# Optimization experiments

Hardware: AMD Instinct MI355X
Metric: run time of the kernel (lower is better)

Reference implementation:

```python
import jax, jax.numpy as jnp
import numpy as np

B, H, W, C = 4, 64, 64, 256
DQK, DV = C // 8, C // 2  # 32, 128


def setup_inputs() -> dict:
    key = jax.random.key(0)
    ks = jax.random.split(key, 5)
    x = jax.random.normal(ks[0], (B, H, W, C), dtype=jnp.float32)
    # 1x1 conv kernels stored as [C_in, C_out] matrices (Glorot-ish scale)
    Wf = jax.random.normal(ks[1], (C, DQK), dtype=jnp.float32) * 0.05
    Wg = jax.random.normal(ks[2], (C, DQK), dtype=jnp.float32) * 0.05
    Wh = jax.random.normal(ks[3], (C, DV), dtype=jnp.float32) * 0.05
    Wv = jax.random.normal(ks[4], (DV, C), dtype=jnp.float32) * 0.05
    return {
        "x": x,
        "Wf": Wf, "bf": jnp.zeros((DQK,), jnp.float32),
        "Wg": Wg, "bg": jnp.zeros((DQK,), jnp.float32),
        "Wh": Wh, "bh": jnp.zeros((DV,), jnp.float32),
        "Wv": Wv, "bv": jnp.zeros((C,), jnp.float32),
    }


def reference(x, Wf, bf, Wg, bg, Wh, bh, Wv, bv):
    b, h, w, c = x.shape
    n = h * w
    xf = x.reshape(b, n, c)                       # flatten spatial dims
    f = xf @ Wf + bf                              # [b, n, dqk] keys
    g = xf @ Wg + bg                              # [b, n, dqk] queries
    v = xf @ Wh + bh                              # [b, n, dv]  values
    s = jnp.einsum('bnd,bmd->bnm', g, f)          # unscaled scores [b, n, n]
    beta = jax.nn.softmax(s, axis=-1)
    o = jnp.einsum('bnm,bmd->bnd', beta, v)       # [b, n, dv]
    o = o @ Wv + bv                               # output 1x1 conv -> [b, n, c]
    out = xf + o                                  # residual
    return out.reshape(b, h, w, c)
```

## Files before the change

kernel.cpp:

```cpp
#include <hip/hip_runtime.h>
#include <hip/hip_bf16.h>
#include <stdint.h>

typedef __attribute__((ext_vector_type(8))) short short8;
typedef __attribute__((ext_vector_type(4))) float f32x4;

#define B_   4
#define N_   4096
#define C_   256
#define DQK  32
#define DV   128
#define NCOL 192
#define QBLK 64
#define KVB  64
#define TOT  (B_*N_)
#define PROWB 144

__device__ __forceinline__ uint16_t f2bf(float f) {
    uint32_t u = __float_as_uint(f);
    u += 0x7fffu + ((u >> 16) & 1u);
    return (uint16_t)(u >> 16);
}

__global__ __launch_bounds__(256) void prep_weights(
    const float* __restrict__ Wf, const float* __restrict__ Wg,
    const float* __restrict__ Wh, const float* __restrict__ Wv,
    uint16_t* __restrict__ WfghT, uint16_t* __restrict__ WvT)
{
    int idx = blockIdx.x * 256 + threadIdx.x;
    if (idx < NCOL * C_) {
        int c = idx / C_, k = idx % C_;
        float v = (c < DQK)   ? Wf[k * DQK + c]
                : (c < 2*DQK) ? Wg[k * DQK + (c - DQK)]
                              : Wh[k * DV  + (c - 2*DQK)];
        WfghT[idx] = f2bf(v);
    }
    int idx2 = idx - NCOL * C_;
    if (idx2 >= 0 && idx2 < C_ * DV) {
        int c = idx2 / DV, k = idx2 % DV;
        WvT[idx2] = f2bf(Wv[k * C_ + c]);
    }
}

__global__ __launch_bounds__(256) void proj_kernel(
    const float* __restrict__ x, const uint16_t* __restrict__ WfghT,
    const float* __restrict__ bf, const float* __restrict__ bg,
    const float* __restrict__ bh,
    uint16_t* __restrict__ fK, uint16_t* __restrict__ gQ,
    uint16_t* __restrict__ vT)
{
    __shared__ __align__(16) uint16_t vlds[128 * 72];
    const int lane = threadIdx.x & 63;
    const int w    = threadIdx.x >> 6;
    const int rb   = blockIdx.x * 64 + w * 16;
    const int lr   = lane & 15, lg = lane >> 4;
    const int arow = rb + lr;

    const f32x4 z = {0.f, 0.f, 0.f, 0.f};
    f32x4 acc[12];
#pragma unroll
    for (int i = 0; i < 12; ++i) acc[i] = z;

#pragma unroll
    for (int kc = 0; kc < 8; ++kc) {
        const float* ap = x + (size_t)arow * C_ + kc * 32 + lg * 8;
        f32x4 u0 = *(const f32x4*)ap;
        f32x4 u1 = *(const f32x4*)(ap + 4);
        short8 a;
        a[0]=(short)f2bf(u0[0]); a[1]=(short)f2bf(u0[1]);
        a[2]=(short)f2bf(u0[2]); a[3]=(short)f2bf(u0[3]);
        a[4]=(short)f2bf(u1[0]); a[5]=(short)f2bf(u1[1]);
        a[6]=(short)f2bf(u1[2]); a[7]=(short)f2bf(u1[3]);
#pragma unroll
        for (int ct = 0; ct < 12; ++ct) {
            short8 b = *(const short8*)(WfghT + (ct*16 + lr) * C_ + kc*32 + lg*8);
            acc[ct] = __builtin_amdgcn_mfma_f32_16x16x32_bf16(a, b, acc[ct], 0, 0, 0);
        }
    }

#pragma unroll
    for (int ct = 0; ct < 12; ++ct) {
        int col = ct * 16 + lr;
        float bias = (col < DQK)   ? bf[col]
                   : (col < 2*DQK) ? bg[col - DQK]
                                   : bh[col - 2*DQK];
#pragma unroll
        for (int i = 0; i < 4; ++i) {
            int row = rb + lg * 4 + i;
            uint16_t h = f2bf(acc[ct][i] + bias);
            if (col < DQK) {
                fK[(size_t)row * DQK + col] = h;
            } else if (col < 2*DQK) {
                gQ[(size_t)row * DQK + (col - DQK)] = h;
            } else {
                int vc = col - 2*DQK;
                int nl = w * 16 + lg * 4 + i;
                vlds[vc * 72 + nl] = h;
            }
        }
    }
    __syncthreads();
    const int rb0   = blockIdx.x * 64;
    const int b_    = rb0 >> 12;
    const int nbase = rb0 & (N_ - 1);
    const int tid   = threadIdx.x;
#pragma unroll
    for (int pass = 0; pass < 4; ++pass) {
        int vc = pass * 32 + (tid >> 3);
        int nl = (tid & 7) * 8;
        short8 vv = *(const short8*)(vlds + vc * 72 + nl);
        *(short8*)(vT + ((size_t)b_ * DV + vc) * N_ + nbase + nl) = vv;
    }
}

template<int S>
__global__ __launch_bounds__(256) void attn_kernel(
    const uint16_t* __restrict__ fK, const uint16_t* __restrict__ gQ,
    const uint16_t* __restrict__ vT,
    float* __restrict__ opart, float* __restrict__ msplit,
    float* __restrict__ lsplit)
{
    __shared__ __align__(16) uint8_t lds[2*4096 + 2*16384 + 4*2304];
    uint8_t* Kl = lds;
    uint8_t* Vl = lds + 2*4096;
    const int lane = threadIdx.x & 63;
    const int w    = threadIdx.x >> 6;
    uint8_t* Pl = lds + 2*4096 + 2*16384 + w * 2304;
    const int lr = lane & 15, lg = lane >> 4;

    const int bid   = blockIdx.x;
    const int xcd   = bid & 7;
    const int b     = xcd >> 1;
    const int t_    = bid >> 3;
    const int s     = t_ >> 5;
    const int qtile = (xcd & 1) * 32 + (t_ & 31);
    const int qbase = qtile * QBLK;
    const int kv0   = s * (N_ / S);
    const int NTS   = 64 / S;

    short8 aq = *(const short8*)(gQ + ((size_t)(b*N_ + qbase + w*16 + lr)) * DQK + lg*8);

    const f32x4 z = {0.f, 0.f, 0.f, 0.f};
    f32x4 oa[8];
#pragma unroll
    for (int i = 0; i < 8; ++i) oa[i] = z;
    float m_run[4] = {-1e30f, -1e30f, -1e30f, -1e30f};
    float l_run[4] = {0.f, 0.f, 0.f, 0.f};

    const uint16_t* fbase = fK + (size_t)b * N_ * DQK;
    const uint16_t* vbase = vT + (size_t)b * DV * N_;

    auto STAGE = [&](int buf, int kbase) {
        {
            int sl  = w * 64 + lane;
            int key = sl >> 2;
            int g   = (sl & 3) ^ ((key >> 1) & 3);
            const uint16_t* src = fbase + (size_t)(kbase + key) * DQK + g * 8;
            __builtin_amdgcn_global_load_lds(
                (const __attribute__((address_space(1))) uint32_t*)src,
                (__attribute__((address_space(3))) uint32_t*)(Kl + buf*4096 + w*1024),
                16, 0, 0);
        }
#pragma unroll
        for (int q = 0; q < 4; ++q) {
            int sl = w * 256 + q * 64 + lane;
            int vc = sl >> 3;
            int ks = (sl & 7) ^ (vc & 7);
            const uint16_t* src = vbase + (size_t)vc * N_ + kbase + ks * 8;
            __builtin_amdgcn_global_load_lds(
                (const __attribute__((address_space(1))) uint32_t*)src,
                (__attribute__((address_space(3))) uint32_t*)(Vl + buf*16384 + (w*256 + q*64)*16),
                16, 0, 0);
        }
    };

    auto COMPUTE = [&](int buf) {
        const uint8_t* Kb = Kl + buf * 4096;
        const uint8_t* Vb = Vl + buf * 16384;
        f32x4 sf[4];
#pragma unroll
        for (int kg = 0; kg < 4; ++kg) {
            int key   = kg * 16 + lr;
            int slotK = key * 4 + (lg ^ ((key >> 1) & 3));
            short8 kb = *(const short8*)(Kb + slotK * 16);
            sf[kg] = __builtin_amdgcn_mfma_f32_16x16x32_bf16(aq, kb, z, 0, 0, 0);
        }
#pragma unroll
        for (int i = 0; i < 4; ++i) {
            float tm = fmaxf(fmaxf(sf[0][i], sf[1][i]), fmaxf(sf[2][i], sf[3][i]));
            tm = fmaxf(tm, __shfl_xor(tm, 1, 16));
            tm = fmaxf(tm, __shfl_xor(tm, 2, 16));
            tm = fmaxf(tm, __shfl_xor(tm, 4, 16));
            tm = fmaxf(tm, __shfl_xor(tm, 8, 16));
            float mn = fmaxf(m_run[i], tm);
            float sc = __expf(m_run[i] - mn);
            m_run[i] = mn;
            float rs = 0.f;
#pragma unroll
            for (int kg = 0; kg < 4; ++kg) {
                float p = __expf(sf[kg][i] - mn);
                sf[kg][i] = p;
                rs += p;
            }
            rs += __shfl_xor(rs, 1, 16);
            rs += __shfl_xor(rs, 2, 16);
            rs += __shfl_xor(rs, 4, 16);
            rs += __shfl_xor(rs, 8, 16);
            l_run[i] = l_run[i] * sc + rs;
#pragma unroll
            for (int ct = 0; ct < 8; ++ct) oa[ct][i] *= sc;
#pragma unroll
            for (int kg = 0; kg < 4; ++kg) {
                *(uint16_t*)(Pl + (lg*4 + i) * PROWB + (kg*16 + lr) * 2) = f2bf(sf[kg][i]);
            }
        }
        __builtin_amdgcn_sched_barrier(0);
        asm volatile("s_waitcnt lgkmcnt(0)" ::: "memory");
        __builtin_amdgcn_sched_barrier(0);
#pragma unroll
        for (int kc = 0; kc < 2; ++kc) {
            short8 pa = *(const short8*)(Pl + lr * PROWB + kc * 64 + lg * 16);
#pragma unroll
            for (int ct = 0; ct < 8; ++ct) {
                int vc    = ct * 16 + lr;
                int ks    = kc * 4 + lg;
                int slotV = vc * 8 + (ks ^ (vc & 7));
                short8 vb = *(const short8*)(Vb + slotV * 16);
                oa[ct] = __builtin_amdgcn_mfma_f32_16x16x32_bf16(pa, vb, oa[ct], 0, 0, 0);
            }
        }
    };

    STAGE(0, kv0);
    for (int t = 0; t < NTS; ++t) {
        if (t + 1 < NTS) {
            STAGE((t + 1) & 1, kv0 + (t + 1) * KVB);
            asm volatile("s_waitcnt vmcnt(5)" ::: "memory");
        } else {
            asm volatile("s_waitcnt vmcnt(0)" ::: "memory");
        }
        asm volatile("s_barrier" ::: "memory");
        COMPUTE(t & 1);
        asm volatile("s_barrier" ::: "memory");
    }

#pragma unroll
    for (int i = 0; i < 4; ++i) {
        int grow = b * N_ + qbase + w * 16 + lg * 4 + i;
        float* op = opart + ((size_t)s * TOT + grow) * DV;
#pragma unroll
        for (int ct = 0; ct < 8; ++ct) {
            op[ct * 16 + lr] = oa[ct][i];
        }
        if (lr == 0) {
            msplit[s * TOT + grow] = m_run[i];
            lsplit[s * TOT + grow] = l_run[i];
        }
    }
}

template<int S>
__global__ __launch_bounds__(256) void out_kernel(
    const float* __restrict__ opart, const float* __restrict__ msplit,
    const float* __restrict__ lsplit, const uint16_t* __restrict__ WvT,
    const float* __restrict__ x, const float* __restrict__ bv,
    float* __restrict__ out)
{
    const int lane = threadIdx.x & 63;
    const int w    = threadIdx.x >> 6;
    const int rb   = blockIdx.x * 64 + w * 16;
    const int lr   = lane & 15, lg = lane >> 4;
    const int row  = rb + lr;

    float wsn[S];
    {
        float ms[S], ls[S];
#pragma unroll
        for (int su = 0; su < S; ++su) {
            ms[su] = msplit[su * TOT + row];
            ls[su] = lsplit[su * TOT + row];
        }
        float mx = -1e30f;
#pragma unroll
        for (int su = 0; su < S; ++su) mx = fmaxf(mx, ms[su]);
        float L = 0.f;
#pragma unroll
        for (int su = 0; su < S; ++su) { wsn[su] = __expf(ms[su] - mx); L += wsn[su] * ls[su]; }
        float inv = 1.f / L;
#pragma unroll
        for (int su = 0; su < S; ++su) wsn[su] *= inv;
    }

    const f32x4 z = {0.f, 0.f, 0.f, 0.f};
    f32x4 acc[16];
#pragma unroll
    for (int i = 0; i < 16; ++i) acc[i] = z;

#pragma unroll
    for (int kc = 0; kc < 4; ++kc) {
        float af[8] = {0.f,0.f,0.f,0.f,0.f,0.f,0.f,0.f};
#pragma unroll
        for (int su = 0; su < S; ++su) {
            const float* ov = opart + ((size_t)su * TOT + row) * DV + kc*32 + lg*8;
            f32x4 o0 = *(const f32x4*)ov;
            f32x4 o1 = *(const f32x4*)(ov + 4);
#pragma unroll
            for (int j = 0; j < 4; ++j) {
                af[j]     += wsn[su] * o0[j];
                af[j + 4] += wsn[su] * o1[j];
            }
        }
        short8 a;
#pragma unroll
        for (int j = 0; j < 8; ++j) a[j] = (short)f2bf(af[j]);
#pragma unroll
        for (int ct = 0; ct < 16; ++ct) {
            short8 bfr = *(const short8*)(WvT + (ct*16 + lr) * DV + kc*32 + lg*8);
            acc[ct] = __builtin_amdgcn_mfma_f32_16x16x32_bf16(a, bfr, acc[ct], 0, 0, 0);
        }
    }
#pragma unroll
    for (int ct = 0; ct < 16; ++ct) {
        int col = ct * 16 + lr;
        float bb = bv[col];
#pragma unroll
        for (int i = 0; i < 4; ++i) {
            size_t idx = (size_t)(rb + lg*4 + i) * C_ + col;
            out[idx] = acc[ct][i] + bb + x[idx];
        }
    }
}

extern "C" void kernel_launch(void* const* d_in, const int* in_sizes, int n_in,
                              void* d_out, int out_size, void* d_ws, size_t ws_size,
                              hipStream_t stream)
{
    const float* x  = (const float*)d_in[0];
    const float* Wf = (const float*)d_in[1];
    const float* bf = (const float*)d_in[2];
    const float* Wg = (const float*)d_in[3];
    const float* bg = (const float*)d_in[4];
    const float* Wh = (const float*)d_in[5];
    const float* bh = (const float*)d_in[6];
    const float* Wv = (const float*)d_in[7];
    const float* bv = (const float*)d_in[8];
    float* out = (float*)d_out;

    const size_t fixed = (size_t)NCOL*C_*2 + (size_t)C_*DV*2
                       + 2*(size_t)TOT*DQK*2 + (size_t)B_*DV*N_*2;
    auto need = [&](size_t S){ return fixed + S*TOT*DV*4 + 2*S*TOT*4; };
    const int S = (ws_size >= need(4)) ? 4 : (ws_size >= need(2)) ? 2 : 1;

    uint8_t* ws = (uint8_t*)d_ws;
    size_t off = 0;
    uint16_t* WfghT = (uint16_t*)(ws + off); off += (size_t)NCOL * C_ * 2;
    uint16_t* WvT   = (uint16_t*)(ws + off); off += (size_t)C_ * DV * 2;
    uint16_t* fK    = (uint16_t*)(ws + off); off += (size_t)TOT * DQK * 2;
    uint16_t* gQ    = (uint16_t*)(ws + off); off += (size_t)TOT * DQK * 2;
    uint16_t* vT    = (uint16_t*)(ws + off); off += (size_t)B_ * DV * N_ * 2;
    float*    opart = (float*)(ws + off);    off += (size_t)S * TOT * DV * 4;
    float*    mspl  = (float*)(ws + off);    off += (size_t)S * TOT * 4;
    float*    lspl  = (float*)(ws + off);    off += (size_t)S * TOT * 4;

    prep_weights<<<320, 256, 0, stream>>>(Wf, Wg, Wh, Wv, WfghT, WvT);
    proj_kernel <<<256, 256, 0, stream>>>(x, WfghT, bf, bg, bh, fK, gQ, vT);
    switch (S) {
    case 4:
        attn_kernel<4><<<1024, 256, 0, stream>>>(fK, gQ, vT, opart, mspl, lspl);
        out_kernel<4> <<<256, 256, 0, stream>>>(opart, mspl, lspl, WvT, x, bv, out);
        break;
    case 2:
        attn_kernel<2><<<512, 256, 0, stream>>>(fK, gQ, vT, opart, mspl, lspl);
        out_kernel<2> <<<256, 256, 0, stream>>>(opart, mspl, lspl, WvT, x, bv, out);
        break;
    default:
        attn_kernel<1><<<256, 256, 0, stream>>>(fK, gQ, vT, opart, mspl, lspl);
        out_kernel<1> <<<256, 256, 0, stream>>>(opart, mspl, lspl, WvT, x, bv, out);
        break;
    }
}
```

Before: 186.8 us.

## Use 8-wave attention blocks sharing K/V staging and split proj/out kernels

The attention kernel now runs 512-thread blocks covering 128 queries, so each staged K/V tile in LDS is reused by eight waves instead of four, halving global K/V traffic per query. Staging work per wave shrinks accordingly and the vmcnt wait is adjusted. The projection kernel is split into separate f/g and v blocks, and the output kernel splits output columns across two blocks, doubling grid sizes for better CU occupancy. The risks are fewer attention blocks per GPU (512 for S=4), higher LDS use per block, and redundant x reads in the split kernels.

```diff
diff --git a/kernel.cpp b/kernel.cpp
--- a/kernel.cpp
+++ b/kernel.cpp
@@ -11,7 +11,6 @@
 #define DQK  32
 #define DV   128
 #define NCOL 192
-#define QBLK 64
 #define KVB  64
 #define TOT  (B_*N_)
 #define PROWB 144
@@ -50,16 +49,18 @@
     uint16_t* __restrict__ vT)
 {
     __shared__ __align__(16) uint16_t vlds[128 * 72];
+    const bool isV = blockIdx.x >= 256;
+    const int bx   = isV ? blockIdx.x - 256 : blockIdx.x;
     const int lane = threadIdx.x & 63;
     const int w    = threadIdx.x >> 6;
-    const int rb   = blockIdx.x * 64 + w * 16;
+    const int rb   = bx * 64 + w * 16;
     const int lr   = lane & 15, lg = lane >> 4;
     const int arow = rb + lr;
 
     const f32x4 z = {0.f, 0.f, 0.f, 0.f};
-    f32x4 acc[12];
-#pragma unroll
-    for (int i = 0; i < 12; ++i) acc[i] = z;
+    f32x4 acc[8];
+#pragma unroll
+    for (int i = 0; i < 8; ++i) acc[i] = z;
 
 #pragma unroll
     for (int kc = 0; kc < 8; ++kc) {
@@ -71,56 +72,68 @@
         a[2]=(short)f2bf(u0[2]); a[3]=(short)f2bf(u0[3]);
         a[4]=(short)f2bf(u1[0]); a[5]=(short)f2bf(u1[1]);
         a[6]=(short)f2bf(u1[2]); a[7]=(short)f2bf(u1[3]);
-#pragma unroll
-        for (int ct = 0; ct < 12; ++ct) {
-            short8 b = *(const short8*)(WfghT + (ct*16 + lr) * C_ + kc*32 + lg*8);
-            acc[ct] = __builtin_amdgcn_mfma_f32_16x16x32_bf16(a, b, acc[ct], 0, 0, 0);
-        }
-    }
-
-#pragma unroll
-    for (int ct = 0; ct < 12; ++ct) {
-        int col = ct * 16 + lr;
-        float bias = (col < DQK)   ? bf[col]
-                   : (col < 2*DQK) ? bg[col - DQK]
-                                   : bh[col - 2*DQK];
-#pragma unroll
-        for (int i = 0; i < 4; ++i) {
-            int row = rb + lg * 4 + i;
-            uint16_t h = f2bf(acc[ct][i] + bias);
-            if (col < DQK) {
-                fK[(size_t)row * DQK + col] = h;
-            } else if (col < 2*DQK) {
-                gQ[(size_t)row * DQK + (col - DQK)] = h;
-            } else {
-                int vc = col - 2*DQK;
+        if (isV) {
+#pragma unroll
+            for (int ct = 0; ct < 8; ++ct) {
+                short8 b = *(const short8*)(WfghT + (64 + ct*16 + lr) * C_ + kc*32 + lg*8);
+                acc[ct] = __builtin_amdgcn_mfma_f32_16x16x32_bf16(a, b, acc[ct], 0, 0, 0);
+            }
+        } else {
+#pragma unroll
+            for (int ct = 0; ct < 4; ++ct) {
+                short8 b = *(const short8*)(WfghT + (ct*16 + lr) * C_ + kc*32 + lg*8);
+                acc[ct] = __builtin_amdgcn_mfma_f32_16x16x32_bf16(a, b, acc[ct], 0, 0, 0);
+            }
+        }
+    }
+
+    if (!isV) {
+#pragma unroll
+        for (int ct = 0; ct < 4; ++ct) {
+            int col = ct * 16 + lr;
+            float bias = (col < DQK) ? bf[col] : bg[col - DQK];
+#pragma unroll
+            for (int i = 0; i < 4; ++i) {
+                int row = rb + lg * 4 + i;
+                uint16_t h = f2bf(acc[ct][i] + bias);
+                if (col < DQK) fK[(size_t)row * DQK + col] = h;
+                else           gQ[(size_t)row * DQK + (col - DQK)] = h;
+            }
+        }
+    } else {
+#pragma unroll
+        for (int ct = 0; ct < 8; ++ct) {
+            int vc = ct * 16 + lr;
+            float bias = bh[vc];
+#pragma unroll
+            for (int i = 0; i < 4; ++i) {
                 int nl = w * 16 + lg * 4 + i;
-                vlds[vc * 72 + nl] = h;
-            }
-        }
-    }
-    __syncthreads();
-    const int rb0   = blockIdx.x * 64;
-    const int b_    = rb0 >> 12;
-    const int nbase = rb0 & (N_ - 1);
-    const int tid   = threadIdx.x;
-#pragma unroll
-    for (int pass = 0; pass < 4; ++pass) {
-        int vc = pass * 32 + (tid >> 3);
-        int nl = (tid & 7) * 8;
-        short8 vv = *(const short8*)(vlds + vc * 72 + nl);
-        *(short8*)(vT + ((size_t)b_ * DV + vc) * N_ + nbase + nl) = vv;
+                vlds[vc * 72 + nl] = f2bf(acc[ct][i] + bias);
+            }
+        }
+        __syncthreads();
+        const int rb0   = bx * 64;
+        const int b_    = rb0 >> 12;
+        const int nbase = rb0 & (N_ - 1);
+        const int tid   = threadIdx.x;
+#pragma unroll
+        for (int pass = 0; pass < 4; ++pass) {
+            int vc = pass * 32 + (tid >> 3);
+            int nl = (tid & 7) * 8;
+            short8 vv = *(const short8*)(vlds + vc * 72 + nl);
+            *(short8*)(vT + ((size_t)b_ * DV + vc) * N_ + nbase + nl) = vv;
+        }
     }
 }
 
 template<int S>
-__global__ __launch_bounds__(256) void attn_kernel(
+__global__ __launch_bounds__(512) void attn_kernel(
     const uint16_t* __restrict__ fK, const uint16_t* __restrict__ gQ,
     const uint16_t* __restrict__ vT,
     float* __restrict__ opart, float* __restrict__ msplit,
     float* __restrict__ lsplit)
 {
-    __shared__ __align__(16) uint8_t lds[2*4096 + 2*16384 + 4*2304];
+    __shared__ __align__(16) uint8_t lds[2*4096 + 2*16384 + 8*2304];
     uint8_t* Kl = lds;
     uint8_t* Vl = lds + 2*4096;
     const int lane = threadIdx.x & 63;
@@ -128,15 +141,15 @@
     uint8_t* Pl = lds + 2*4096 + 2*16384 + w * 2304;
     const int lr = lane & 15, lg = lane >> 4;
 
-    const int bid   = blockIdx.x;
-    const int xcd   = bid & 7;
-    const int b     = xcd >> 1;
-    const int t_    = bid >> 3;
-    const int s     = t_ >> 5;
-    const int qtile = (xcd & 1) * 32 + (t_ & 31);
-    const int qbase = qtile * QBLK;
-    const int kv0   = s * (N_ / S);
-    const int NTS   = 64 / S;
+    const int bid  = blockIdx.x;
+    const int xcd  = bid & 7;
+    const int b    = xcd >> 1;
+    const int rest = bid >> 3;
+    const int s    = rest >> 4;
+    const int qtile= (xcd & 1) * 16 + (rest & 15);
+    const int qbase= qtile * 128;
+    const int kv0  = s * (N_ / S);
+    const int NTS  = 64 / S;
 
     short8 aq = *(const short8*)(gQ + ((size_t)(b*N_ + qbase + w*16 + lr)) * DQK + lg*8);
 
@@ -151,25 +164,25 @@
     const uint16_t* vbase = vT + (size_t)b * DV * N_;
 
     auto STAGE = [&](int buf, int kbase) {
-        {
-            int sl  = w * 64 + lane;
+        if (lane < 32) {
+            int sl  = w * 32 + lane;
             int key = sl >> 2;
             int g   = (sl & 3) ^ ((key >> 1) & 3);
             const uint16_t* src = fbase + (size_t)(kbase + key) * DQK + g * 8;
             __builtin_amdgcn_global_load_lds(
                 (const __attribute__((address_space(1))) uint32_t*)src,
-                (__attribute__((address_space(3))) uint32_t*)(Kl + buf*4096 + w*1024),
+                (__attribute__((address_space(3))) uint32_t*)(Kl + buf*4096 + w*512),
                 16, 0, 0);
         }
 #pragma unroll
-        for (int q = 0; q < 4; ++q) {
-            int sl = w * 256 + q * 64 + lane;
+        for (int q = 0; q < 2; ++q) {
+            int sl = w * 128 + q * 64 + lane;
             int vc = sl >> 3;
             int ks = (sl & 7) ^ (vc & 7);
             const uint16_t* src = vbase + (size_t)vc * N_ + kbase + ks * 8;
             __builtin_amdgcn_global_load_lds(
                 (const __attribute__((address_space(1))) uint32_t*)src,
-                (__attribute__((address_space(3))) uint32_t*)(Vl + buf*16384 + (w*256 + q*64)*16),
+                (__attribute__((address_space(3))) uint32_t*)(Vl + buf*16384 + (w*128 + q*64)*16),
                 16, 0, 0);
         }
     };
@@ -235,7 +248,7 @@
     for (int t = 0; t < NTS; ++t) {
         if (t + 1 < NTS) {
             STAGE((t + 1) & 1, kv0 + (t + 1) * KVB);
-            asm volatile("s_waitcnt vmcnt(5)" ::: "memory");
+            asm volatile("s_waitcnt vmcnt(3)" ::: "memory");
         } else {
             asm volatile("s_waitcnt vmcnt(0)" ::: "memory");
         }
@@ -268,7 +281,8 @@
 {
     const int lane = threadIdx.x & 63;
     const int w    = threadIdx.x >> 6;
-    const int rb   = blockIdx.x * 64 + w * 16;
+    const int rb   = (blockIdx.x >> 1) * 64 + w * 16;
+    const int ch   = blockIdx.x & 1;
     const int lr   = lane & 15, lg = lane >> 4;
     const int row  = rb + lr;
 
@@ -292,9 +306,9 @@
     }
 
     const f32x4 z = {0.f, 0.f, 0.f, 0.f};
-    f32x4 acc[16];
-#pragma unroll
-    for (int i = 0; i < 16; ++i) acc[i] = z;
+    f32x4 acc[8];
+#pragma unroll
+    for (int i = 0; i < 8; ++i) acc[i] = z;
 
 #pragma unroll
     for (int kc = 0; kc < 4; ++kc) {
@@ -314,14 +328,15 @@
 #pragma unroll
         for (int j = 0; j < 8; ++j) a[j] = (short)f2bf(af[j]);
 #pragma unroll
-        for (int ct = 0; ct < 16; ++ct) {
-            short8 bfr = *(const short8*)(WvT + (ct*16 + lr) * DV + kc*32 + lg*8);
+        for (int ct = 0; ct < 8; ++ct) {
+            int col = ch * 128 + ct * 16 + lr;
+            short8 bfr = *(const short8*)(WvT + (size_t)col * DV + kc*32 + lg*8);
             acc[ct] = __builtin_amdgcn_mfma_f32_16x16x32_bf16(a, bfr, acc[ct], 0, 0, 0);
         }
     }
 #pragma unroll
-    for (int ct = 0; ct < 16; ++ct) {
-        int col = ct * 16 + lr;
+    for (int ct = 0; ct < 8; ++ct) {
+        int col = ch * 128 + ct * 16 + lr;
         float bb = bv[col];
 #pragma unroll
         for (int i = 0; i < 4; ++i) {
@@ -363,19 +378,19 @@
     float*    lspl  = (float*)(ws + off);    off += (size_t)S * TOT * 4;
 
     prep_weights<<<320, 256, 0, stream>>>(Wf, Wg, Wh, Wv, WfghT, WvT);
-    proj_kernel <<<256, 256, 0, stream>>>(x, WfghT, bf, bg, bh, fK, gQ, vT);
+    proj_kernel <<<512, 256, 0, stream>>>(x, WfghT, bf, bg, bh, fK, gQ, vT);
     switch (S) {
     case 4:
-        attn_kernel<4><<<1024, 256, 0, stream>>>(fK, gQ, vT, opart, mspl, lspl);
-        out_kernel<4> <<<256, 256, 0, stream>>>(opart, mspl, lspl, WvT, x, bv, out);
+        attn_kernel<4><<<512, 512, 0, stream>>>(fK, gQ, vT, opart, mspl, lspl);
+        out_kernel<4> <<<512, 256, 0, stream>>>(opart, mspl, lspl, WvT, x, bv, out);
         break;
     case 2:
-        attn_kernel<2><<<512, 256, 0, stream>>>(fK, gQ, vT, opart, mspl, lspl);
-        out_kernel<2> <<<256, 256, 0, stream>>>(opart, mspl, lspl, WvT, x, bv, out);
+        attn_kernel<2><<<256, 512, 0, stream>>>(fK, gQ, vT, opart, mspl, lspl);
+        out_kernel<2> <<<512, 256, 0, stream>>>(opart, mspl, lspl, WvT, x, bv, out);
         break;
     default:
-        attn_kernel<1><<<256, 256, 0, stream>>>(fK, gQ, vT, opart, mspl, lspl);
-        out_kernel<1> <<<256, 256, 0, stream>>>(opart, mspl, lspl, WvT, x, bv, out);
+        attn_kernel<1><<<128, 512, 0, stream>>>(fK, gQ, vT, opart, mspl, lspl);
+        out_kernel<1> <<<512, 256, 0, stream>>>(opart, mspl, lspl, WvT, x, bv, out);
         break;
     }
 }
```

New measurement: 173.1 us. 7.3% less time.
